# Performance work log

Hardware: AMD Instinct MI355X
Metric: run time of the kernel (lower is better)

## Reference

```python
import jax, jax.numpy as jnp
import numpy as np

D = 1024
H = 16
DH = D // H  # 64
SCALE = DH ** (-0.5)

def setup_inputs() -> dict:
    key = jax.random.key(0)
    k1, k2, k3, k4, k5 = jax.random.split(key, 5)
    x = jax.random.normal(k1, (4, 2048, D), dtype=jnp.float32)
    w_qkv = jax.random.normal(k2, (D, 3 * D), dtype=jnp.float32) * (D ** -0.5)
    b_qkv = jax.random.normal(k3, (3 * D,), dtype=jnp.float32) * 0.02
    w_out = jax.random.normal(k4, (D, D), dtype=jnp.float32) * (D ** -0.5)
    b_out = jax.random.normal(k5, (D,), dtype=jnp.float32) * 0.02
    return {"x": x, "w_qkv": w_qkv, "b_qkv": b_qkv, "w_out": w_out, "b_out": b_out}

def reference(x, w_qkv, b_qkv, w_out, b_out):
    B, S, C = x.shape
    qkv = x @ w_qkv + b_qkv                          # [B,S,3D]
    qkv = qkv.reshape(B, S, 3, H, DH)
    qkv = jnp.transpose(qkv, (0, 3, 2, 1, 4))        # [B,H,3,S,DH]
    q, k, v = qkv[:, :, 0], qkv[:, :, 1], qkv[:, :, 2]
    q = q * SCALE
    scores = jnp.einsum('bhqd,bhkd->bhqk', q, k)     # [B,H,S,S]
    attn = jax.nn.softmax(scores.astype(jnp.float32), axis=-1).astype(scores.dtype)
    out = jnp.einsum('bhqk,bhkd->bhqd', attn, v)     # [B,H,S,DH]
    out = jnp.transpose(out, (0, 2, 1, 3)).reshape(B, S, C)
    return out @ w_out + b_out
```

## Files before the change

kernel.cpp:

```cpp
#include <hip/hip_runtime.h>

#define D_ 1024
#define H_ 16
#define DH_ 64
#define S_ 2048
#define B_ 4
#define N_ (B_*S_)
#define M3_ 3072
#define QSC_ 0.18033688011112042f

typedef _Float16 f16;
typedef _Float16 f16x8 __attribute__((ext_vector_type(8)));
typedef _Float16 f16x4 __attribute__((ext_vector_type(4)));
typedef _Float16 f16x2 __attribute__((ext_vector_type(2)));
typedef __fp16   h16x2 __attribute__((ext_vector_type(2)));
typedef float    f32x4 __attribute__((ext_vector_type(4)));

typedef __attribute__((address_space(1))) void gvoid;
typedef __attribute__((address_space(3))) void lvoid;

__device__ __forceinline__ void gl16(const f16* g, f16* l) {
    __builtin_amdgcn_global_load_lds((gvoid*)g, (lvoid*)l, 16, 0, 0);
}

__device__ __forceinline__ f16x2 pk_cvt(float a, float b) {
#if __has_builtin(__builtin_amdgcn_cvt_pkrtz)
    h16x2 t = __builtin_amdgcn_cvt_pkrtz(a, b);
    return __builtin_bit_cast(f16x2, t);
#else
    f16x2 r; r[0] = (f16)a; r[1] = (f16)b; return r;
#endif
}

__device__ __forceinline__ float dot2acc(f16x2 a, float acc) {
#if __has_builtin(__builtin_amdgcn_fdot2)
    h16x2 one; one[0] = (__fp16)1.f; one[1] = (__fp16)1.f;
    return __builtin_amdgcn_fdot2(__builtin_bit_cast(h16x2, a), one, acc, false);
#else
    return acc + (float)a[0] + (float)a[1];
#endif
}

__global__ __launch_bounds__(256) void cvt_x_kernel(const float* __restrict__ in,
                                                    f16* __restrict__ out) {
    size_t i = ((size_t)blockIdx.x * 256 + threadIdx.x) * 4;
    float4 f = *reinterpret_cast<const float4*>(in + i);
    f16x4 o;
    o[0] = (f16)f.x; o[1] = (f16)f.y; o[2] = (f16)f.z; o[3] = (f16)f.w;
    *reinterpret_cast<f16x4*>(out + i) = o;
}

__global__ __launch_bounds__(256) void wt_cvt_kernel(const float* __restrict__ in,
                                                     f16* __restrict__ out,
                                                     int K, int Nc) {
    __shared__ float tile[32][33];
    int tx = threadIdx.x & 31, ty = threadIdx.x >> 5;
    int c = blockIdx.x * 32 + tx;
    #pragma unroll
    for (int i = 0; i < 4; i++) {
        int r = blockIdx.y * 32 + ty + i * 8;
        tile[ty + i * 8][tx] = in[(size_t)r * Nc + c];
    }
    __syncthreads();
    #pragma unroll
    for (int i = 0; i < 4; i++) {
        int r2 = blockIdx.x * 32 + ty + i * 8;
        int c2 = blockIdx.y * 32 + tx;
        out[(size_t)r2 * K + c2] = (f16)tile[tx][ty + i * 8];
    }
}

__global__ __launch_bounds__(256) void gemm_qkv_kernel(
        const f16* __restrict__ A, const f16* __restrict__ Bt,
        const float* __restrict__ bias,
        f16* __restrict__ qo, f16* __restrict__ ko, f16* __restrict__ vo) {
    __shared__ __align__(16) f16 As[128 * 32];
    __shared__ __align__(16) f16 Bs[128 * 32];
    const int tid  = threadIdx.x;
    const int lane = tid & 63, w = tid >> 6;
    const int quad = lane >> 4, lrow = lane & 15;
    const int wm = (w & 1) * 64, wn = (w >> 1) * 64;
    const int n0 = blockIdx.x * 128, m0 = blockIdx.y * 128;

    f32x4 acc[4][4];
    #pragma unroll
    for (int i = 0; i < 4; i++)
        #pragma unroll
        for (int j = 0; j < 4; j++) acc[i][j] = {0.f, 0.f, 0.f, 0.f};

    const int ar0 = tid >> 2, ap0 = tid & 3;
    const f16* Ag0 = A  + (size_t)(n0 + ar0) * D_ + ap0 * 8;
    const f16* Ag1 = Ag0 + (size_t)64 * D_;
    const f16* Bg0 = Bt + (size_t)(m0 + ar0) * D_ + ap0 * 8;
    const f16* Bg1 = Bg0 + (size_t)64 * D_;
    f16* Asl = As + tid * 8;
    f16* Bsl = Bs + tid * 8;

    for (int kt = 0; kt < D_ / 32; kt++) {
        gl16(Ag0 + kt * 32, Asl);
        gl16(Ag1 + kt * 32, Asl + 64 * 32);
        gl16(Bg0 + kt * 32, Bsl);
        gl16(Bg1 + kt * 32, Bsl + 64 * 32);
        __syncthreads();
        f16x8 af[4], bf[4];
        #pragma unroll
        for (int i = 0; i < 4; i++)
            af[i] = *reinterpret_cast<const f16x8*>(&As[(wm + i * 16 + lrow) * 32 + quad * 8]);
        #pragma unroll
        for (int j = 0; j < 4; j++)
            bf[j] = *reinterpret_cast<const f16x8*>(&Bs[(wn + j * 16 + lrow) * 32 + quad * 8]);
        #pragma unroll
        for (int i = 0; i < 4; i++)
            #pragma unroll
            for (int j = 0; j < 4; j++)
                acc[i][j] = __builtin_amdgcn_mfma_f32_16x16x32_f16(af[i], bf[j], acc[i][j], 0, 0, 0);
        __syncthreads();
    }

    #pragma unroll
    for (int j = 0; j < 4; j++) {
        int m   = m0 + wn + j * 16 + lrow;
        int sec = m >> 10;
        int hd  = m & 1023;
        int hh  = hd >> 6, d = hd & 63;
        float bb = bias[m];
        f16* dst = (sec == 0) ? qo : (sec == 1) ? ko : vo;
        float sc = (sec == 0) ? QSC_ : 1.0f;
        #pragma unroll
        for (int i = 0; i < 4; i++) {
            #pragma unroll
            for (int r = 0; r < 4; r++) {
                int n = n0 + wm + i * 16 + quad * 4 + r;
                int bidx = n >> 11, s = n & 2047;
                dst[(((size_t)(bidx * H_ + hh)) * S_ + s) * DH_ + d] =
                    (f16)((acc[i][j][r] + bb) * sc);
            }
        }
    }
}

__global__ __launch_bounds__(256) void transpose_v_kernel(const f16* __restrict__ v,
                                                          f16* __restrict__ vT) {
    __shared__ f16 t[64][65];
    int bh = blockIdx.y, s0 = blockIdx.x * 64;
    const f16* src = v + ((size_t)bh * S_ + s0) * DH_;
    #pragma unroll
    for (int i = 0; i < 16; i++) {
        int idx = threadIdx.x + i * 256;
        int s = idx >> 6, d = idx & 63;
        t[s][d] = src[s * 64 + d];
    }
    __syncthreads();
    f16* dst = vT + (size_t)bh * DH_ * S_ + s0;
    #pragma unroll
    for (int i = 0; i < 16; i++) {
        int idx = threadIdx.x + i * 256;
        int d = idx >> 6, s = idx & 63;
        dst[(size_t)d * S_ + s] = t[s][d];
    }
}

__global__ __launch_bounds__(256) void attn_kernel(
        const f16* __restrict__ q, const f16* __restrict__ k,
        const f16* __restrict__ vT, f16* __restrict__ ctx) {
    __shared__ __align__(16) f16 Ks[128 * 72];
    __shared__ __align__(16) f16 Vs[64 * 136];
    const int tid  = threadIdx.x;
    const int lane = tid & 63, w = tid >> 6;
    const int quad = lane >> 4, lrow = lane & 15;
    const int bh = blockIdx.y;
    const int b  = bh >> 4, h = bh & 15;
    const int q0 = blockIdx.x * 256;
    const f16* qb = q  + (size_t)bh * S_ * DH_;
    const f16* kb = k  + (size_t)bh * S_ * DH_;
    const f16* vb = vT + (size_t)bh * DH_ * S_;

    f16x8 qf[4][2];
    #pragma unroll
    for (int f = 0; f < 4; f++)
        #pragma unroll
        for (int hf = 0; hf < 2; hf++)
            qf[f][hf] = *reinterpret_cast<const f16x8*>(
                qb + (size_t)(q0 + w * 64 + f * 16 + lrow) * DH_ + hf * 32 + quad * 8);

    float l_i[4] = {0.f, 0.f, 0.f, 0.f};
    f32x4 ot[4][4];
    #pragma unroll
    for (int f = 0; f < 4; f++)
        #pragma unroll
        for (int dj = 0; dj < 4; dj++) ot[f][dj] = {0.f, 0.f, 0.f, 0.f};

    f16x8 krg[4], vrg[4];
    #pragma unroll
    for (int i = 0; i < 4; i++) {
        int ch = tid + i * 256;
        krg[i] = *reinterpret_cast<const f16x8*>(kb + (size_t)(ch >> 3) * DH_ + (ch & 7) * 8);
        vrg[i] = *reinterpret_cast<const f16x8*>(vb + (size_t)(ch >> 4) * S_ + (ch & 15) * 8);
    }

    for (int kt = 0; kt < S_ / 128; kt++) {
        #pragma unroll
        for (int i = 0; i < 4; i++) {
            int ch = tid + i * 256;
            *reinterpret_cast<f16x8*>(&Ks[(ch >> 3) * 72 + (ch & 7) * 8]) = krg[i];
            *reinterpret_cast<f16x8*>(&Vs[(ch >> 4) * 136 + (ch & 15) * 8]) = vrg[i];
        }
        __syncthreads();
        if (kt + 1 < S_ / 128) {
            const int kv1 = (kt + 1) * 128;
            #pragma unroll
            for (int i = 0; i < 4; i++) {
                int ch = tid + i * 256;
                krg[i] = *reinterpret_cast<const f16x8*>(kb + (size_t)(kv1 + (ch >> 3)) * DH_ + (ch & 7) * 8);
                vrg[i] = *reinterpret_cast<const f16x8*>(vb + (size_t)(ch >> 4) * S_ + kv1 + (ch & 15) * 8);
            }
        }

        #pragma unroll
        for (int mb = 0; mb < 8; mb++) {
            f16x8 kf0 = *reinterpret_cast<const f16x8*>(&Ks[(mb * 16 + lrow) * 72 + quad * 8]);
            f16x8 kf1 = *reinterpret_cast<const f16x8*>(&Ks[(mb * 16 + lrow) * 72 + 32 + quad * 8]);
            f32x4 st[4];
            #pragma unroll
            for (int f = 0; f < 4; f++) {
                f32x4 t = {0.f, 0.f, 0.f, 0.f};
                t = __builtin_amdgcn_mfma_f32_16x16x32_f16(kf0, qf[f][0], t, 0, 0, 0);
                t = __builtin_amdgcn_mfma_f32_16x16x32_f16(kf1, qf[f][1], t, 0, 0, 0);
                st[f] = t;
            }
            f16x4 pfv[4];
            #pragma unroll
            for (int f = 0; f < 4; f++) {
                f16x2 lo = pk_cvt(__builtin_amdgcn_exp2f(st[f][0]),
                                  __builtin_amdgcn_exp2f(st[f][1]));
                f16x2 hi = pk_cvt(__builtin_amdgcn_exp2f(st[f][2]),
                                  __builtin_amdgcn_exp2f(st[f][3]));
                l_i[f] = dot2acc(lo, l_i[f]);
                l_i[f] = dot2acc(hi, l_i[f]);
                pfv[f][0] = lo[0]; pfv[f][1] = lo[1];
                pfv[f][2] = hi[0]; pfv[f][3] = hi[1];
            }
            #pragma unroll
            for (int dj = 0; dj < 4; dj++) {
                f16x4 vf = *reinterpret_cast<const f16x4*>(
                    &Vs[(dj * 16 + lrow) * 136 + mb * 16 + quad * 4]);
                #pragma unroll
                for (int f = 0; f < 4; f++)
                    ot[f][dj] = __builtin_amdgcn_mfma_f32_16x16x16f16(vf, pfv[f], ot[f][dj], 0, 0, 0);
            }
        }
        __syncthreads();
    }

    #pragma unroll
    for (int f = 0; f < 4; f++) {
        float l = l_i[f];
        l += __shfl_xor(l, 16);
        l += __shfl_xor(l, 32);
        float inv = 1.0f / l;
        int qrow = q0 + w * 64 + f * 16 + lrow;
        #pragma unroll
        for (int dj = 0; dj < 4; dj++) {
            f16x4 o;
            #pragma unroll
            for (int r = 0; r < 4; r++) o[r] = (f16)(ot[f][dj][r] * inv);
            *reinterpret_cast<f16x4*>(
                &ctx[((size_t)(b * S_ + qrow)) * D_ + h * DH_ + dj * 16 + quad * 4]) = o;
        }
    }
}

__global__ __launch_bounds__(256) void gemm_out_kernel(
        const f16* __restrict__ A, const f16* __restrict__ Bt,
        const float* __restrict__ bias, float* __restrict__ out) {
    __shared__ __align__(16) f16 As[128 * 32];
    __shared__ __align__(16) f16 Bs[128 * 32];
    const int tid  = threadIdx.x;
    const int lane = tid & 63, w = tid >> 6;
    const int quad = lane >> 4, lrow = lane & 15;
    const int wm = (w & 1) * 64, wn = (w >> 1) * 64;
    const int n0 = blockIdx.x * 128, m0 = blockIdx.y * 128;

    f32x4 acc[4][4];
    #pragma unroll
    for (int i = 0; i < 4; i++)
        #pragma unroll
        for (int j = 0; j < 4; j++) acc[i][j] = {0.f, 0.f, 0.f, 0.f};

    const int ar0 = tid >> 2, ap0 = tid & 3;
    const f16* Ag0 = A  + (size_t)(n0 + ar0) * D_ + ap0 * 8;
    const f16* Ag1 = Ag0 + (size_t)64 * D_;
    const f16* Bg0 = Bt + (size_t)(m0 + ar0) * D_ + ap0 * 8;
    const f16* Bg1 = Bg0 + (size_t)64 * D_;
    f16* Asl = As + tid * 8;
    f16* Bsl = Bs + tid * 8;

    for (int kt = 0; kt < D_ / 32; kt++) {
        gl16(Ag0 + kt * 32, Asl);
        gl16(Ag1 + kt * 32, Asl + 64 * 32);
        gl16(Bg0 + kt * 32, Bsl);
        gl16(Bg1 + kt * 32, Bsl + 64 * 32);
        __syncthreads();
        f16x8 af[4], bf[4];
        #pragma unroll
        for (int i = 0; i < 4; i++)
            af[i] = *reinterpret_cast<const f16x8*>(&As[(wm + i * 16 + lrow) * 32 + quad * 8]);
        #pragma unroll
        for (int j = 0; j < 4; j++)
            bf[j] = *reinterpret_cast<const f16x8*>(&Bs[(wn + j * 16 + lrow) * 32 + quad * 8]);
        #pragma unroll
        for (int i = 0; i < 4; i++)
            #pragma unroll
            for (int j = 0; j < 4; j++)
                acc[i][j] = __builtin_amdgcn_mfma_f32_16x16x32_f16(af[i], bf[j], acc[i][j], 0, 0, 0);
        __syncthreads();
    }

    #pragma unroll
    for (int j = 0; j < 4; j++) {
        int m = m0 + wn + j * 16 + lrow;
        float bb = bias[m];
        #pragma unroll
        for (int i = 0; i < 4; i++)
            #pragma unroll
            for (int r = 0; r < 4; r++) {
                int n = n0 + wm + i * 16 + quad * 4 + r;
                out[(size_t)n * D_ + m] = acc[i][j][r] + bb;
            }
    }
}

extern "C" void kernel_launch(void* const* d_in, const int* in_sizes, int n_in,
                              void* d_out, int out_size, void* d_ws, size_t ws_size,
                              hipStream_t stream) {
    (void)in_sizes; (void)n_in; (void)out_size; (void)ws_size;
    const float* x     = (const float*)d_in[0];
    const float* w_qkv = (const float*)d_in[1];
    const float* b_qkv = (const float*)d_in[2];
    const float* w_out = (const float*)d_in[3];
    const float* b_out = (const float*)d_in[4];
    float* out = (float*)d_out;

    char* ws = (char*)d_ws;
    const size_t MB = 1024 * 1024;
    f16* xb    = (f16*)(ws);
    f16* wqkvT = (f16*)(ws + 16 * MB);
    f16* woutT = (f16*)(ws + 22 * MB);
    f16* qs    = (f16*)(ws + 24 * MB);
    f16* kk    = (f16*)(ws + 40 * MB);
    f16* vv    = (f16*)(ws + 56 * MB);
    f16* vTb   = (f16*)(ws + 72 * MB);
    f16* ctx   = xb;

    cvt_x_kernel<<<(N_ * D_) / (256 * 4), 256, 0, stream>>>(x, xb);
    wt_cvt_kernel<<<dim3(M3_ / 32, D_ / 32), 256, 0, stream>>>(w_qkv, wqkvT, D_, M3_);
    wt_cvt_kernel<<<dim3(D_ / 32, D_ / 32), 256, 0, stream>>>(w_out, woutT, D_, D_);
    gemm_qkv_kernel<<<dim3(N_ / 128, M3_ / 128), 256, 0, stream>>>(xb, wqkvT, b_qkv, qs, kk, vv);
    transpose_v_kernel<<<dim3(S_ / 64, B_ * H_), 256, 0, stream>>>(vv, vTb);
    attn_kernel<<<dim3(S_ / 256, B_ * H_), 256, 0, stream>>>(qs, kk, vTb, ctx);
    gemm_out_kernel<<<dim3(N_ / 128, D_ / 128), 256, 0, stream>>>(ctx, woutT, b_out, out);
}
```

Measured before the change: 297.5 us.

## Fuse V transpose into QKV GEMM epilogue and use K=32 MFMA for PV

The QKV GEMM epilogue now writes V directly in transposed [bh, d, s] layout using 4-wide f16 stores, which removes the separate transpose_v kernel and its global round trip. In the attention kernel, K rows are permuted when stored to LDS so that two 16-key score blocks can be packed into one 8-wide P fragment. The PV product then uses 16x16x32 MFMAs instead of 16x16x16, halving the MFMA count for that step. The permutation has to line up exactly with the P register layout, so correctness depends on that index mapping being right.

```diff
diff --git a/kernel.cpp b/kernel.cpp
--- a/kernel.cpp
+++ b/kernel.cpp
@@ -73,7 +73,7 @@
 __global__ __launch_bounds__(256) void gemm_qkv_kernel(
         const f16* __restrict__ A, const f16* __restrict__ Bt,
         const float* __restrict__ bias,
-        f16* __restrict__ qo, f16* __restrict__ ko, f16* __restrict__ vo) {
+        f16* __restrict__ qo, f16* __restrict__ ko, f16* __restrict__ vTo) {
     __shared__ __align__(16) f16 As[128 * 32];
     __shared__ __align__(16) f16 Bs[128 * 32];
     const int tid  = threadIdx.x;
@@ -124,39 +124,31 @@
         int hd  = m & 1023;
         int hh  = hd >> 6, d = hd & 63;
         float bb = bias[m];
-        f16* dst = (sec == 0) ? qo : (sec == 1) ? ko : vo;
-        float sc = (sec == 0) ? QSC_ : 1.0f;
-        #pragma unroll
-        for (int i = 0; i < 4; i++) {
-            #pragma unroll
-            for (int r = 0; r < 4; r++) {
-                int n = n0 + wm + i * 16 + quad * 4 + r;
+        if (sec == 2) {
+            #pragma unroll
+            for (int i = 0; i < 4; i++) {
+                int n = n0 + wm + i * 16 + quad * 4;
                 int bidx = n >> 11, s = n & 2047;
-                dst[(((size_t)(bidx * H_ + hh)) * S_ + s) * DH_ + d] =
-                    (f16)((acc[i][j][r] + bb) * sc);
-            }
-        }
-    }
-}
-
-__global__ __launch_bounds__(256) void transpose_v_kernel(const f16* __restrict__ v,
-                                                          f16* __restrict__ vT) {
-    __shared__ f16 t[64][65];
-    int bh = blockIdx.y, s0 = blockIdx.x * 64;
-    const f16* src = v + ((size_t)bh * S_ + s0) * DH_;
-    #pragma unroll
-    for (int i = 0; i < 16; i++) {
-        int idx = threadIdx.x + i * 256;
-        int s = idx >> 6, d = idx & 63;
-        t[s][d] = src[s * 64 + d];
-    }
-    __syncthreads();
-    f16* dst = vT + (size_t)bh * DH_ * S_ + s0;
-    #pragma unroll
-    for (int i = 0; i < 16; i++) {
-        int idx = threadIdx.x + i * 256;
-        int d = idx >> 6, s = idx & 63;
-        dst[(size_t)d * S_ + s] = t[s][d];
+                f16x4 o;
+                #pragma unroll
+                for (int r = 0; r < 4; r++) o[r] = (f16)(acc[i][j][r] + bb);
+                *reinterpret_cast<f16x4*>(
+                    &vTo[(((size_t)(bidx * H_ + hh)) * DH_ + d) * S_ + s]) = o;
+            }
+        } else {
+            f16* dst = (sec == 0) ? qo : ko;
+            float sc = (sec == 0) ? QSC_ : 1.0f;
+            #pragma unroll
+            for (int i = 0; i < 4; i++) {
+                #pragma unroll
+                for (int r = 0; r < 4; r++) {
+                    int n = n0 + wm + i * 16 + quad * 4 + r;
+                    int bidx = n >> 11, s = n & 2047;
+                    dst[(((size_t)(bidx * H_ + hh)) * S_ + s) * DH_ + d] =
+                        (f16)((acc[i][j][r] + bb) * sc);
+                }
+            }
+        }
     }
 }
 
@@ -190,20 +182,29 @@
         #pragma unroll
         for (int dj = 0; dj < 4; dj++) ot[f][dj] = {0.f, 0.f, 0.f, 0.f};
 
+    int kslot[4], kpart[4], vrow[4], vpart[4];
+    #pragma unroll
+    for (int i = 0; i < 4; i++) {
+        int ch = tid + i * 256;
+        int g = ch >> 3, jj = g & 7, qd = (g >> 3) & 3;
+        kslot[i] = (g & ~31) + ((jj >> 2) << 4) + (qd << 2) + (jj & 3);
+        kpart[i] = ch & 7;
+        vrow[i] = ch >> 4; vpart[i] = ch & 15;
+    }
+
     f16x8 krg[4], vrg[4];
     #pragma unroll
     for (int i = 0; i < 4; i++) {
         int ch = tid + i * 256;
         krg[i] = *reinterpret_cast<const f16x8*>(kb + (size_t)(ch >> 3) * DH_ + (ch & 7) * 8);
-        vrg[i] = *reinterpret_cast<const f16x8*>(vb + (size_t)(ch >> 4) * S_ + (ch & 15) * 8);
+        vrg[i] = *reinterpret_cast<const f16x8*>(vb + (size_t)vrow[i] * S_ + vpart[i] * 8);
     }
 
     for (int kt = 0; kt < S_ / 128; kt++) {
         #pragma unroll
         for (int i = 0; i < 4; i++) {
-            int ch = tid + i * 256;
-            *reinterpret_cast<f16x8*>(&Ks[(ch >> 3) * 72 + (ch & 7) * 8]) = krg[i];
-            *reinterpret_cast<f16x8*>(&Vs[(ch >> 4) * 136 + (ch & 15) * 8]) = vrg[i];
+            *reinterpret_cast<f16x8*>(&Ks[kslot[i] * 72 + kpart[i] * 8]) = krg[i];
+            *reinterpret_cast<f16x8*>(&Vs[vrow[i] * 136 + vpart[i] * 8]) = vrg[i];
         }
         __syncthreads();
         if (kt + 1 < S_ / 128) {
@@ -212,41 +213,40 @@
             for (int i = 0; i < 4; i++) {
                 int ch = tid + i * 256;
                 krg[i] = *reinterpret_cast<const f16x8*>(kb + (size_t)(kv1 + (ch >> 3)) * DH_ + (ch & 7) * 8);
-                vrg[i] = *reinterpret_cast<const f16x8*>(vb + (size_t)(ch >> 4) * S_ + kv1 + (ch & 15) * 8);
-            }
-        }
-
-        #pragma unroll
-        for (int mb = 0; mb < 8; mb++) {
-            f16x8 kf0 = *reinterpret_cast<const f16x8*>(&Ks[(mb * 16 + lrow) * 72 + quad * 8]);
-            f16x8 kf1 = *reinterpret_cast<const f16x8*>(&Ks[(mb * 16 + lrow) * 72 + 32 + quad * 8]);
-            f32x4 st[4];
-            #pragma unroll
-            for (int f = 0; f < 4; f++) {
-                f32x4 t = {0.f, 0.f, 0.f, 0.f};
-                t = __builtin_amdgcn_mfma_f32_16x16x32_f16(kf0, qf[f][0], t, 0, 0, 0);
-                t = __builtin_amdgcn_mfma_f32_16x16x32_f16(kf1, qf[f][1], t, 0, 0, 0);
-                st[f] = t;
-            }
-            f16x4 pfv[4];
-            #pragma unroll
-            for (int f = 0; f < 4; f++) {
-                f16x2 lo = pk_cvt(__builtin_amdgcn_exp2f(st[f][0]),
-                                  __builtin_amdgcn_exp2f(st[f][1]));
-                f16x2 hi = pk_cvt(__builtin_amdgcn_exp2f(st[f][2]),
-                                  __builtin_amdgcn_exp2f(st[f][3]));
-                l_i[f] = dot2acc(lo, l_i[f]);
-                l_i[f] = dot2acc(hi, l_i[f]);
-                pfv[f][0] = lo[0]; pfv[f][1] = lo[1];
-                pfv[f][2] = hi[0]; pfv[f][3] = hi[1];
+                vrg[i] = *reinterpret_cast<const f16x8*>(vb + (size_t)vrow[i] * S_ + kv1 + vpart[i] * 8);
+            }
+        }
+
+        #pragma unroll
+        for (int t = 0; t < 4; t++) {
+            f16x8 p8[4];
+            #pragma unroll
+            for (int half = 0; half < 2; half++) {
+                int mb = 2 * t + half;
+                f16x8 kf0 = *reinterpret_cast<const f16x8*>(&Ks[(mb * 16 + lrow) * 72 + quad * 8]);
+                f16x8 kf1 = *reinterpret_cast<const f16x8*>(&Ks[(mb * 16 + lrow) * 72 + 32 + quad * 8]);
+                #pragma unroll
+                for (int f = 0; f < 4; f++) {
+                    f32x4 st = {0.f, 0.f, 0.f, 0.f};
+                    st = __builtin_amdgcn_mfma_f32_16x16x32_f16(kf0, qf[f][0], st, 0, 0, 0);
+                    st = __builtin_amdgcn_mfma_f32_16x16x32_f16(kf1, qf[f][1], st, 0, 0, 0);
+                    f16x2 lo = pk_cvt(__builtin_amdgcn_exp2f(st[0]),
+                                      __builtin_amdgcn_exp2f(st[1]));
+                    f16x2 hi = pk_cvt(__builtin_amdgcn_exp2f(st[2]),
+                                      __builtin_amdgcn_exp2f(st[3]));
+                    l_i[f] = dot2acc(lo, l_i[f]);
+                    l_i[f] = dot2acc(hi, l_i[f]);
+                    p8[f][half * 4 + 0] = lo[0]; p8[f][half * 4 + 1] = lo[1];
+                    p8[f][half * 4 + 2] = hi[0]; p8[f][half * 4 + 3] = hi[1];
+                }
             }
             #pragma unroll
             for (int dj = 0; dj < 4; dj++) {
-                f16x4 vf = *reinterpret_cast<const f16x4*>(
-                    &Vs[(dj * 16 + lrow) * 136 + mb * 16 + quad * 4]);
+                f16x8 vf = *reinterpret_cast<const f16x8*>(
+                    &Vs[(dj * 16 + lrow) * 136 + t * 32 + quad * 8]);
                 #pragma unroll
                 for (int f = 0; f < 4; f++)
-                    ot[f][dj] = __builtin_amdgcn_mfma_f32_16x16x16f16(vf, pfv[f], ot[f][dj], 0, 0, 0);
+                    ot[f][dj] = __builtin_amdgcn_mfma_f32_16x16x32_f16(vf, p8[f], ot[f][dj], 0, 0, 0);
             }
         }
         __syncthreads();
@@ -348,15 +348,13 @@
     f16* woutT = (f16*)(ws + 22 * MB);
     f16* qs    = (f16*)(ws + 24 * MB);
     f16* kk    = (f16*)(ws + 40 * MB);
-    f16* vv    = (f16*)(ws + 56 * MB);
     f16* vTb   = (f16*)(ws + 72 * MB);
     f16* ctx   = xb;
 
     cvt_x_kernel<<<(N_ * D_) / (256 * 4), 256, 0, stream>>>(x, xb);
     wt_cvt_kernel<<<dim3(M3_ / 32, D_ / 32), 256, 0, stream>>>(w_qkv, wqkvT, D_, M3_);
     wt_cvt_kernel<<<dim3(D_ / 32, D_ / 32), 256, 0, stream>>>(w_out, woutT, D_, D_);
-    gemm_qkv_kernel<<<dim3(N_ / 128, M3_ / 128), 256, 0, stream>>>(xb, wqkvT, b_qkv, qs, kk, vv);
-    transpose_v_kernel<<<dim3(S_ / 64, B_ * H_), 256, 0, stream>>>(vv, vTb);
+    gemm_qkv_kernel<<<dim3(N_ / 128, M3_ / 128), 256, 0, stream>>>(xb, wqkvT, b_qkv, qs, kk, vTb);
     attn_kernel<<<dim3(S_ / 256, B_ * H_), 256, 0, stream>>>(qs, kk, vTb, ctx);
     gemm_out_kernel<<<dim3(N_ / 128, D_ / 128), 256, 0, stream>>>(ctx, woutT, b_out, out);
 }
```

New measurement: 274.9 us. 1.08x faster.
